# Optimization experiments

Measured on AMD Instinct MI355X. Metric: run time of the kernel, lower is better.

## Reference

```python
import jax, jax.numpy as jnp
import numpy as np

B, CIN, COUT, K, STRIDE, PAD = 32, 64, 128, 3, 1, 1
IN_H, IN_W = 112, 112


def setup_inputs() -> dict:
    key = jax.random.key(0)
    k1, k2 = jax.random.split(key)
    # x_padded already has `PAD` rows/cols of zeros on each side, as in the torch module
    x = jax.random.normal(k1, (B, CIN, IN_H, IN_W), dtype=jnp.float32)
    x_padded = jnp.pad(x, ((0, 0), (0, 0), (PAD, PAD), (PAD, PAD)))
    weight = jax.random.normal(k2, (COUT, CIN, K, K), dtype=jnp.float32) * 0.1
    bias = jnp.zeros((COUT,), dtype=jnp.float32)
    return {
        "x_padded": x_padded,
        "in_height": IN_H,
        "in_width": IN_W,
        "weight": weight,
        "bias": bias,
    }


def reference(x_padded, in_height, in_width, weight, bias):
    # CustomConv2D.custom_conv2d: direct conv over the pre-padded input.
    # out[b,o,h,w] = sum_{i,kh,kw} x_padded[b,i,h*s+kh,w*s+kw] * weight[o,i,kh,kw] + bias[o]
    out = jax.lax.conv_general_dilated(
        x_padded, weight,
        window_strides=(STRIDE, STRIDE),
        padding="VALID",  # padding already applied to x_padded
        dimension_numbers=("NCHW", "OIHW", "NCHW"),
    )
    return out + bias[None, :, None, None]
```

## Files before the change

kernel.cpp:

```cpp
#include <hip/hip_runtime.h>

typedef __attribute__((ext_vector_type(8))) short short8;
typedef __attribute__((ext_vector_type(4))) float f32x4;
typedef __attribute__((ext_vector_type(4))) unsigned int u32x4;
typedef unsigned short u16;
typedef unsigned int u32;

#define XH 114
#define XW 114
#define CINC 64
#define COUT 128
#define OH 112
#define OW 112
#define NB 32
#define KTOT 576
#define ROWB 14592

static __device__ __forceinline__ u16 f2bf(float f) {
    u32 x = __float_as_uint(f);
    u32 r = (x + 0x7fffu + ((x >> 16) & 1u)) >> 16;
    return (u16)r;
}

#define MFMA16(a, b, c) __builtin_amdgcn_mfma_f32_16x16x32_bf16((a), (b), (c), 0, 0, 0)

static __device__ __forceinline__ void gload16(const void* g, void* l) {
    __builtin_amdgcn_global_load_lds(
        (const __attribute__((address_space(1))) unsigned int*)g,
        (__attribute__((address_space(3))) unsigned int*)l, 16, 0, 0);
}


__global__ __launch_bounds__(256) void prep(const float* __restrict__ x,
                                            const float* __restrict__ w,
                                            u16* __restrict__ xb,
                                            u16* __restrict__ wbf) {
    const int tid = threadIdx.x;
    const int blk = blockIdx.x;
    if (blk >= NB * XH) {
        int i = (blk - NB * XH) * 256 + tid;
        int o = i / KTOT;
        int rem = i - o * KTOT;
        int khkw = rem >> 6;
        int ci = rem & 63;
        wbf[i] = f2bf(w[(o * CINC + ci) * 9 + khkw]);
        return;
    }
    __shared__ u16 tile[XW * 70];
    const int b = blk / XH;
    const int h = blk - b * XH;

    #pragma unroll
    for (int it = 0; it < 15; ++it) {
        int idx = it * 256 + tid;
        if (idx < 32 * XW) {
            int cp = idx / XW;
            int w_ = idx - cp * XW;
            const float* s0 = x + ((size_t)(b * CINC + 2 * cp) * XH + h) * XW + w_;
            float a = s0[0];
            float c = s0[XH * XW];
            u32 pk = (u32)f2bf(a) | ((u32)f2bf(c) << 16);
            *(u32*)&tile[w_ * 70 + 2 * cp] = pk;
        }
    }
    __syncthreads();

    u16* dstrow = xb + (size_t)(b * XH + h) * (XW * CINC);
    #pragma unroll
    for (int p2 = 0; p2 < 4; ++p2) {
        int task = p2 * 256 + tid;
        if (task < XW * 8) {
            int w_ = task >> 3;
            int c8 = task & 7;
            const u32* s = (const u32*)&tile[w_ * 70 + c8 * 8];
            u32x4 v = {s[0], s[1], s[2], s[3]};
            int slot = c8 ^ ((2 * h + w_) & 7);
            *(u32x4*)(dstrow + w_ * CINC + slot * 8) = v;
        }
    }
}

__global__ __launch_bounds__(256, 2) void conv_ring(const u16* __restrict__ xb,
                                                    const u16* __restrict__ wbf,
                                                    const float* __restrict__ bias,
                                                    float* __restrict__ out) {
    __shared__ u16 lds[4 * XW * CINC];
    char* ldsc = (char*)lds;

    const int tid  = threadIdx.x;
    const int lane = tid & 63;
    const int wv   = tid >> 6;
    const int l16  = lane & 15;
    const int lhi  = lane >> 4;

    int bidx = blockIdx.x;
    { int xcd = bidx & 7; bidx = xcd * 64 + (bidx >> 3); }
    const int bb = bidx >> 4;
    const int h0 = (bidx & 15) * 7;

    const u16* wrow0 = wbf + (wv * 32 + l16) * KTOT + lhi * 8;
    const u16* wrow1 = wrow0 + 16 * KTOT;
    short8 areg0[18], areg1[18];
    #pragma unroll
    for (int t = 0; t < 18; ++t) {
        areg0[t] = *(const short8*)(wrow0 + t * 32);
        areg1[t] = *(const short8*)(wrow1 + t * 32);
    }
    const float bv0 = bias[wv * 32 + l16];
    const float bv1 = bias[wv * 32 + 16 + l16];

    auto STAGE = [&](int hin) {
        const char* src = (const char*)(xb + (size_t)(bb * XH + hin) * (XW * CINC));
        char* dst = ldsc + (hin & 3) * ROWB;
        #pragma unroll
        for (int it = 0; it < 4; ++it) {
            const int c = it * 4 + wv;
            const int off = c * 1024;
            if (c < 14) {
                gload16(src + off + lane * 16, dst + off);
            } else if (c == 14) {
                if (lane < 16) gload16(src + off + lane * 16, dst + off);
            }
        }
    };

    STAGE(h0); STAGE(h0 + 1); STAGE(h0 + 2);
    __builtin_amdgcn_sched_barrier(0);
    asm volatile("s_waitcnt vmcnt(0) lgkmcnt(0)" ::: "memory");
    __builtin_amdgcn_sched_barrier(0);
    __builtin_amdgcn_s_barrier();

    const f32x4 zero = {0.f, 0.f, 0.f, 0.f};

    #pragma unroll 1
    for (int i = 0; i < 7; ++i) {
        const int hrow = h0 + i;
        if (i < 6) STAGE(hrow + 3);

        f32x4 acc[2][7];
        #pragma unroll
        for (int mf = 0; mf < 2; ++mf)
            #pragma unroll
            for (int nf = 0; nf < 7; ++nf) acc[mf][nf] = zero;

        #pragma unroll
        for (int tt = 0; tt < 9; ++tt) {
            const int kh = tt / 3;
            const int kw = tt - kh * 3;
            const int hin = hrow + kh;
            const int sb  = (hin & 3) * ROWB;
            const int hash = (2 * hin + kw + l16) & 7;
            const int ba0 = sb + ((kw + l16) << 7) + ((lhi ^ hash) << 4);

            #pragma unroll
            for (int nf = 0; nf < 7; ++nf) {
                short8 bf = *(const short8*)(ldsc + ba0 + nf * 2048);
                acc[0][nf] = MFMA16(bf, areg0[2 * tt], acc[0][nf]);
                acc[1][nf] = MFMA16(bf, areg1[2 * tt], acc[1][nf]);
            }
            #pragma unroll
            for (int nf = 0; nf < 7; ++nf) {
                short8 bf = *(const short8*)(ldsc + (ba0 ^ 0x40) + nf * 2048);
                acc[0][nf] = MFMA16(bf, areg0[2 * tt + 1], acc[0][nf]);
                acc[1][nf] = MFMA16(bf, areg1[2 * tt + 1], acc[1][nf]);
            }
        }

        #pragma unroll
        for (int mf = 0; mf < 2; ++mf) {
            const int o = wv * 32 + mf * 16 + l16;
            const float bv = mf ? bv1 : bv0;
            float* po = out + ((size_t)bb * COUT + o) * (OH * OW) + hrow * OW;
            #pragma unroll
            for (int nf = 0; nf < 7; ++nf) {
                f32x4 v = acc[mf][nf];
                v[0] += bv; v[1] += bv; v[2] += bv; v[3] += bv;
                *(f32x4*)(po + nf * 16 + lhi * 4) = v;
            }
        }

        __builtin_amdgcn_sched_barrier(0);
        asm volatile("s_waitcnt vmcnt(14) lgkmcnt(0)" ::: "memory");
        __builtin_amdgcn_sched_barrier(0);
        __builtin_amdgcn_s_barrier();
    }
}


#define BK 32
#define NSTEP 18
#define LDB 40

__global__ __launch_bounds__(256) void wcvt_ident(const float* __restrict__ w,
                                                  u16* __restrict__ wbf) {
    int i = blockIdx.x * 256 + threadIdx.x;
    if (i < COUT * KTOT) wbf[i] = f2bf(w[i]);
}

__global__ __launch_bounds__(256) void conv_fb(const float* __restrict__ x,
                                               const u16* __restrict__ wbf,
                                               const float* __restrict__ bias,
                                               float* __restrict__ out) {
    __shared__ u16 ldsB[OW * LDB];
    const int tid = threadIdx.x;
    int bid = blockIdx.x;
    { int xcd = bid & 7; bid = xcd * 448 + (bid >> 3); }
    const int b = bid / OH;
    const int h = bid - b * OH;
    const float* xbp = x + (size_t)b * (CINC * XH * XW);
    float* outb = out + (size_t)b * (COUT * OH * OW) + h * OW;
    const int lane = tid & 63, wv = tid >> 6, l16 = lane & 15, lhi = lane >> 4;
    const int m0 = wv * 32;
    const int sk = tid >> 3, sn0 = (tid & 7) * 14;
    f32x4 acc[2][7];
    const f32x4 zero = {0.f, 0.f, 0.f, 0.f};
    #pragma unroll
    for (int i = 0; i < 2; ++i)
        #pragma unroll
        for (int j = 0; j < 7; ++j) acc[i][j] = zero;
    for (int t = 0; t < NSTEP; ++t) {
        const int kg = t * BK + sk;
        const int ci = kg / 9;
        const int r9 = kg - ci * 9;
        const int kh = r9 / 3, kw = r9 - (r9 / 3) * 3;
        const float* src = xbp + ((size_t)ci * XH + (h + kh)) * XW + kw + sn0;
        __syncthreads();
        #pragma unroll
        for (int i = 0; i < 14; ++i) ldsB[(sn0 + i) * LDB + sk] = f2bf(src[i]);
        __syncthreads();
        short8 afrag[2];
        #pragma unroll
        for (int mf = 0; mf < 2; ++mf)
            afrag[mf] = *(const short8*)(wbf + (m0 + mf * 16 + l16) * KTOT + t * BK + lhi * 8);
        #pragma unroll
        for (int nf = 0; nf < 7; ++nf) {
            short8 bfrag = *(const short8*)&ldsB[(nf * 16 + l16) * LDB + lhi * 8];
            acc[0][nf] = MFMA16(afrag[0], bfrag, acc[0][nf]);
            acc[1][nf] = MFMA16(afrag[1], bfrag, acc[1][nf]);
        }
    }
    #pragma unroll
    for (int mf = 0; mf < 2; ++mf)
        #pragma unroll
        for (int j = 0; j < 4; ++j) {
            const int o = m0 + mf * 16 + lhi * 4 + j;
            const float bv = bias[o];
            #pragma unroll
            for (int nf = 0; nf < 7; ++nf)
                outb[(size_t)o * (OH * OW) + nf * 16 + l16] = acc[mf][nf][j] + bv;
        }
}

extern "C" void kernel_launch(void* const* d_in, const int* in_sizes, int n_in,
                              void* d_out, int out_size, void* d_ws, size_t ws_size,
                              hipStream_t stream) {
    const float* x    = (const float*)d_in[0];
    const float* w    = (const float*)d_in[3];
    const float* bias = (const float*)d_in[4];
    float* out = (float*)d_out;

    const size_t WBYTES = (size_t)COUT * KTOT * 2;
    const size_t XBYTES = (size_t)NB * XH * XW * CINC * 2;
    if (ws_size >= WBYTES + XBYTES) {
        u16* wbf = (u16*)d_ws;
        u16* xb  = (u16*)((char*)d_ws + WBYTES);
        prep<<<NB * XH + (COUT * KTOT) / 256, 256, 0, stream>>>(x, w, xb, wbf);
        conv_ring<<<512, 256, 0, stream>>>(xb, wbf, bias, out);
    } else {
        u16* wbf = (u16*)d_ws;
        wcvt_ident<<<(COUT * KTOT + 255) / 256, 256, 0, stream>>>(w, wbf);
        conv_fb<<<NB * OH, 256, 0, stream>>>(x, wbf, bias, out);
    }
}
```

Baseline: 110.5 us.

## Shrink LDS ring to three rows and split rows across more blocks

Reduces the LDS row ring from four buffers to three by issuing the next row's load after the kh=0 phase finishes reading the oldest buffer, guarded by an extra barrier. The grid grows from 512 to 768 blocks, each handling 5 or 4 output rows instead of 7, to improve load balance across CUs and let smaller LDS use raise occupancy. The cost is an extra barrier per output row, more redundant halo row loads and weight register preloads per block, and modulo-3 indexing.

```diff
diff --git a/kernel.cpp b/kernel.cpp
--- a/kernel.cpp
+++ b/kernel.cpp
@@ -80,11 +80,11 @@
     }
 }
 
-__global__ __launch_bounds__(256, 2) void conv_ring(const u16* __restrict__ xb,
-                                                    const u16* __restrict__ wbf,
-                                                    const float* __restrict__ bias,
-                                                    float* __restrict__ out) {
-    __shared__ u16 lds[4 * XW * CINC];
+__global__ __launch_bounds__(256, 2) void conv_ring3(const u16* __restrict__ xb,
+                                                     const u16* __restrict__ wbf,
+                                                     const float* __restrict__ bias,
+                                                     float* __restrict__ out) {
+    __shared__ u16 lds[3 * XW * CINC];
     char* ldsc = (char*)lds;
 
     const int tid  = threadIdx.x;
@@ -94,9 +94,11 @@
     const int lhi  = lane >> 4;
 
     int bidx = blockIdx.x;
-    { int xcd = bidx & 7; bidx = xcd * 64 + (bidx >> 3); }
-    const int bb = bidx >> 4;
-    const int h0 = (bidx & 15) * 7;
+    { int xcd = bidx & 7; bidx = xcd * 96 + (bidx >> 3); }
+    const int bb  = bidx / 24;
+    const int grp = bidx - bb * 24;
+    const int h0  = grp < 16 ? grp * 5 : 80 + (grp - 16) * 4;
+    const int cnt = grp < 16 ? 5 : 4;
 
     const u16* wrow0 = wbf + (wv * 32 + l16) * KTOT + lhi * 8;
     const u16* wrow1 = wrow0 + 16 * KTOT;
@@ -111,7 +113,7 @@
 
     auto STAGE = [&](int hin) {
         const char* src = (const char*)(xb + (size_t)(bb * XH + hin) * (XW * CINC));
-        char* dst = ldsc + (hin & 3) * ROWB;
+        char* dst = ldsc + (hin % 3) * ROWB;
         #pragma unroll
         for (int it = 0; it < 4; ++it) {
             const int c = it * 4 + wv;
@@ -133,9 +135,8 @@
     const f32x4 zero = {0.f, 0.f, 0.f, 0.f};
 
     #pragma unroll 1
-    for (int i = 0; i < 7; ++i) {
+    for (int i = 0; i < cnt; ++i) {
         const int hrow = h0 + i;
-        if (i < 6) STAGE(hrow + 3);
 
         f32x4 acc[2][7];
         #pragma unroll
@@ -143,28 +144,39 @@
             #pragma unroll
             for (int nf = 0; nf < 7; ++nf) acc[mf][nf] = zero;
 
-        #pragma unroll
-        for (int tt = 0; tt < 9; ++tt) {
-            const int kh = tt / 3;
-            const int kw = tt - kh * 3;
+        auto PHASE = [&](int kh) {
             const int hin = hrow + kh;
-            const int sb  = (hin & 3) * ROWB;
-            const int hash = (2 * hin + kw + l16) & 7;
-            const int ba0 = sb + ((kw + l16) << 7) + ((lhi ^ hash) << 4);
-
-            #pragma unroll
-            for (int nf = 0; nf < 7; ++nf) {
-                short8 bf = *(const short8*)(ldsc + ba0 + nf * 2048);
-                acc[0][nf] = MFMA16(bf, areg0[2 * tt], acc[0][nf]);
-                acc[1][nf] = MFMA16(bf, areg1[2 * tt], acc[1][nf]);
+            const int sb  = (hin % 3) * ROWB;
+            #pragma unroll
+            for (int kw = 0; kw < 3; ++kw) {
+                const int tt = kh * 3 + kw;
+                const int hash = (2 * hin + kw + l16) & 7;
+                const int ba0 = sb + ((kw + l16) << 7) + ((lhi ^ hash) << 4);
+                #pragma unroll
+                for (int nf = 0; nf < 7; ++nf) {
+                    short8 bf = *(const short8*)(ldsc + ba0 + nf * 2048);
+                    acc[0][nf] = MFMA16(bf, areg0[2 * tt], acc[0][nf]);
+                    acc[1][nf] = MFMA16(bf, areg1[2 * tt], acc[1][nf]);
+                }
+                #pragma unroll
+                for (int nf = 0; nf < 7; ++nf) {
+                    short8 bf = *(const short8*)(ldsc + (ba0 ^ 0x40) + nf * 2048);
+                    acc[0][nf] = MFMA16(bf, areg0[2 * tt + 1], acc[0][nf]);
+                    acc[1][nf] = MFMA16(bf, areg1[2 * tt + 1], acc[1][nf]);
+                }
             }
-            #pragma unroll
-            for (int nf = 0; nf < 7; ++nf) {
-                short8 bf = *(const short8*)(ldsc + (ba0 ^ 0x40) + nf * 2048);
-                acc[0][nf] = MFMA16(bf, areg0[2 * tt + 1], acc[0][nf]);
-                acc[1][nf] = MFMA16(bf, areg1[2 * tt + 1], acc[1][nf]);
-            }
-        }
+        };
+
+        PHASE(0);
+
+        __builtin_amdgcn_sched_barrier(0);
+        asm volatile("s_waitcnt lgkmcnt(0)" ::: "memory");
+        __builtin_amdgcn_sched_barrier(0);
+        __builtin_amdgcn_s_barrier();
+        if (i < cnt - 1) STAGE(hrow + 3);
+
+        PHASE(1);
+        PHASE(2);
 
         #pragma unroll
         for (int mf = 0; mf < 2; ++mf) {
@@ -265,7 +277,7 @@
         u16* wbf = (u16*)d_ws;
         u16* xb  = (u16*)((char*)d_ws + WBYTES);
         prep<<<NB * XH + (COUT * KTOT) / 256, 256, 0, stream>>>(x, w, xb, wbf);
-        conv_ring<<<512, 256, 0, stream>>>(xb, wbf, bias, out);
+        conv_ring3<<<768, 256, 0, stream>>>(xb, wbf, bias, out);
     } else {
         u16* wbf = (u16*)d_ws;
         wcvt_ident<<<(COUT * KTOT + 255) / 256, 256, 0, stream>>>(w, wbf);
```

Measured after the change: 125.6 us. +13.7%, slower.

## Fuse fp32-to-bf16 NHWC input conversion into conv kernel, drop prep pass

Applied to the files above, without the earlier changes.

Removes the separate prep kernel that wrote a bf16 channel-last, swizzled copy of the input to workspace. The conv kernel now loads fp32 NCHW rows directly into registers, converts them to bf16 and writes them swizzled into the LDS ring. The next row's global loads are issued before the MFMA loop and stored to LDS after it, so load latency overlaps compute. This avoids the intermediate global write and re-read, at the cost of more VGPRs, more scattered 4-byte LDS stores, and conversion ALU work inside the conv kernel.

```diff
diff --git a/kernel.cpp b/kernel.cpp
--- a/kernel.cpp
+++ b/kernel.cpp
@@ -2,7 +2,6 @@
 
 typedef __attribute__((ext_vector_type(8))) short short8;
 typedef __attribute__((ext_vector_type(4))) float f32x4;
-typedef __attribute__((ext_vector_type(4))) unsigned int u32x4;
 typedef unsigned short u16;
 typedef unsigned int u32;
 
@@ -24,63 +23,17 @@
 
 #define MFMA16(a, b, c) __builtin_amdgcn_mfma_f32_16x16x32_bf16((a), (b), (c), 0, 0, 0)
 
-static __device__ __forceinline__ void gload16(const void* g, void* l) {
-    __builtin_amdgcn_global_load_lds(
-        (const __attribute__((address_space(1))) unsigned int*)g,
-        (__attribute__((address_space(3))) unsigned int*)l, 16, 0, 0);
-}
-
-
-__global__ __launch_bounds__(256) void prep(const float* __restrict__ x,
-                                            const float* __restrict__ w,
-                                            u16* __restrict__ xb,
-                                            u16* __restrict__ wbf) {
-    const int tid = threadIdx.x;
-    const int blk = blockIdx.x;
-    if (blk >= NB * XH) {
-        int i = (blk - NB * XH) * 256 + tid;
-        int o = i / KTOT;
-        int rem = i - o * KTOT;
-        int khkw = rem >> 6;
-        int ci = rem & 63;
-        wbf[i] = f2bf(w[(o * CINC + ci) * 9 + khkw]);
-        return;
-    }
-    __shared__ u16 tile[XW * 70];
-    const int b = blk / XH;
-    const int h = blk - b * XH;
-
-    #pragma unroll
-    for (int it = 0; it < 15; ++it) {
-        int idx = it * 256 + tid;
-        if (idx < 32 * XW) {
-            int cp = idx / XW;
-            int w_ = idx - cp * XW;
-            const float* s0 = x + ((size_t)(b * CINC + 2 * cp) * XH + h) * XW + w_;
-            float a = s0[0];
-            float c = s0[XH * XW];
-            u32 pk = (u32)f2bf(a) | ((u32)f2bf(c) << 16);
-            *(u32*)&tile[w_ * 70 + 2 * cp] = pk;
-        }
-    }
-    __syncthreads();
-
-    u16* dstrow = xb + (size_t)(b * XH + h) * (XW * CINC);
-    #pragma unroll
-    for (int p2 = 0; p2 < 4; ++p2) {
-        int task = p2 * 256 + tid;
-        if (task < XW * 8) {
-            int w_ = task >> 3;
-            int c8 = task & 7;
-            const u32* s = (const u32*)&tile[w_ * 70 + c8 * 8];
-            u32x4 v = {s[0], s[1], s[2], s[3]};
-            int slot = c8 ^ ((2 * h + w_) & 7);
-            *(u32x4*)(dstrow + w_ * CINC + slot * 8) = v;
-        }
-    }
-}
-
-__global__ __launch_bounds__(256, 2) void conv_ring(const u16* __restrict__ xb,
+__global__ __launch_bounds__(256) void wcvt_reord(const float* __restrict__ w,
+                                                  u16* __restrict__ wbf) {
+    int i = blockIdx.x * 256 + threadIdx.x;
+    int o = i / KTOT;
+    int rem = i - o * KTOT;
+    int khkw = rem >> 6;
+    int ci = rem & 63;
+    wbf[i] = f2bf(w[(o * CINC + ci) * 9 + khkw]);
+}
+
+__global__ __launch_bounds__(256, 2) void conv_fuse(const float* __restrict__ x,
                                                     const u16* __restrict__ wbf,
                                                     const float* __restrict__ bias,
                                                     float* __restrict__ out) {
@@ -97,6 +50,12 @@
     { int xcd = bidx & 7; bidx = xcd * 64 + (bidx >> 3); }
     const int bb = bidx >> 4;
     const int h0 = (bidx & 15) * 7;
+
+    const int scp = tid & 31;
+    const int sws = tid >> 5;
+    const float* xbase = x + ((size_t)(bb * CINC + 2 * scp) * XH) * XW + sws * 16;
+    const int slotb = scp >> 2;
+    const int cilo  = ((2 * scp) & 7) << 1;
 
     const u16* wrow0 = wbf + (wv * 32 + l16) * KTOT + lhi * 8;
     const u16* wrow1 = wrow0 + 16 * KTOT;
@@ -109,25 +68,41 @@
     const float bv0 = bias[wv * 32 + l16];
     const float bv1 = bias[wv * 32 + 16 + l16];
 
-    auto STAGE = [&](int hin) {
-        const char* src = (const char*)(xb + (size_t)(bb * XH + hin) * (XW * CINC));
+    #pragma unroll 1
+    for (int r = 0; r < 3; ++r) {
+        const int hin = h0 + r;
+        const float* p0 = xbase + (size_t)hin * XW;
+        const float* p1 = p0 + XH * XW;
         char* dst = ldsc + (hin & 3) * ROWB;
-        #pragma unroll
-        for (int it = 0; it < 4; ++it) {
-            const int c = it * 4 + wv;
-            const int off = c * 1024;
-            if (c < 14) {
-                gload16(src + off + lane * 16, dst + off);
-            } else if (c == 14) {
-                if (lane < 16) gload16(src + off + lane * 16, dst + off);
-            }
-        }
-    };
-
-    STAGE(h0); STAGE(h0 + 1); STAGE(h0 + 2);
-    __builtin_amdgcn_sched_barrier(0);
-    asm volatile("s_waitcnt vmcnt(0) lgkmcnt(0)" ::: "memory");
-    __builtin_amdgcn_sched_barrier(0);
+        const int hb = 2 * hin;
+        if (sws < 7) {
+            f32x4 s0[4], s1[4];
+            #pragma unroll
+            for (int k = 0; k < 4; ++k) { s0[k] = *(const f32x4*)(p0 + k * 4);
+                                          s1[k] = *(const f32x4*)(p1 + k * 4); }
+            asm volatile("s_waitcnt vmcnt(0)" ::: "memory");
+            #pragma unroll
+            for (int k = 0; k < 4; ++k)
+                #pragma unroll
+                for (int e = 0; e < 4; ++e) {
+                    const int w = sws * 16 + k * 4 + e;
+                    u32 pk = (u32)f2bf(s0[k][e]) | ((u32)f2bf(s1[k][e]) << 16);
+                    const int swz = slotb ^ ((hb + w) & 7);
+                    *(u32*)(dst + ((w << 7) | (swz << 4) | cilo)) = pk;
+                }
+        } else {
+            float a0 = p0[0], a1 = p0[1], b0_ = p1[0], b1_ = p1[1];
+            asm volatile("s_waitcnt vmcnt(0)" ::: "memory");
+            #pragma unroll
+            for (int e = 0; e < 2; ++e) {
+                const int w = 112 + e;
+                u32 pk = (u32)f2bf(e ? a1 : a0) | ((u32)f2bf(e ? b1_ : b0_) << 16);
+                const int swz = slotb ^ ((hb + w) & 7);
+                *(u32*)(dst + ((w << 7) | (swz << 4) | cilo)) = pk;
+            }
+        }
+    }
+    asm volatile("s_waitcnt lgkmcnt(0)" ::: "memory");
     __builtin_amdgcn_s_barrier();
 
     const f32x4 zero = {0.f, 0.f, 0.f, 0.f};
@@ -135,7 +110,21 @@
     #pragma unroll 1
     for (int i = 0; i < 7; ++i) {
         const int hrow = h0 + i;
-        if (i < 6) STAGE(hrow + 3);
+
+        f32x4 s0[4], s1[4];
+        float ta0 = 0.f, ta1 = 0.f, tb0 = 0.f, tb1 = 0.f;
+        if (i < 6) {
+            const float* p0 = xbase + (size_t)(hrow + 3) * XW;
+            const float* p1 = p0 + XH * XW;
+            if (sws < 7) {
+                #pragma unroll
+                for (int k = 0; k < 4; ++k) { s0[k] = *(const f32x4*)(p0 + k * 4);
+                                              s1[k] = *(const f32x4*)(p1 + k * 4); }
+            } else {
+                ta0 = p0[0]; ta1 = p0[1]; tb0 = p1[0]; tb1 = p1[1];
+            }
+        }
+        __builtin_amdgcn_sched_barrier(0);
 
         f32x4 acc[2][7];
         #pragma unroll
@@ -144,25 +133,52 @@
             for (int nf = 0; nf < 7; ++nf) acc[mf][nf] = zero;
 
         #pragma unroll
-        for (int tt = 0; tt < 9; ++tt) {
-            const int kh = tt / 3;
-            const int kw = tt - kh * 3;
+        for (int kh = 0; kh < 3; ++kh) {
             const int hin = hrow + kh;
             const int sb  = (hin & 3) * ROWB;
-            const int hash = (2 * hin + kw + l16) & 7;
-            const int ba0 = sb + ((kw + l16) << 7) + ((lhi ^ hash) << 4);
-
-            #pragma unroll
-            for (int nf = 0; nf < 7; ++nf) {
-                short8 bf = *(const short8*)(ldsc + ba0 + nf * 2048);
-                acc[0][nf] = MFMA16(bf, areg0[2 * tt], acc[0][nf]);
-                acc[1][nf] = MFMA16(bf, areg1[2 * tt], acc[1][nf]);
-            }
-            #pragma unroll
-            for (int nf = 0; nf < 7; ++nf) {
-                short8 bf = *(const short8*)(ldsc + (ba0 ^ 0x40) + nf * 2048);
-                acc[0][nf] = MFMA16(bf, areg0[2 * tt + 1], acc[0][nf]);
-                acc[1][nf] = MFMA16(bf, areg1[2 * tt + 1], acc[1][nf]);
+            #pragma unroll
+            for (int kw = 0; kw < 3; ++kw) {
+                const int tt = kh * 3 + kw;
+                const int hash = (2 * hin + kw + l16) & 7;
+                const int ba0 = sb + ((kw + l16) << 7) + ((lhi ^ hash) << 4);
+                #pragma unroll
+                for (int nf = 0; nf < 7; ++nf) {
+                    short8 bf = *(const short8*)(ldsc + ba0 + nf * 2048);
+                    acc[0][nf] = MFMA16(bf, areg0[2 * tt], acc[0][nf]);
+                    acc[1][nf] = MFMA16(bf, areg1[2 * tt], acc[1][nf]);
+                }
+                #pragma unroll
+                for (int nf = 0; nf < 7; ++nf) {
+                    short8 bf = *(const short8*)(ldsc + (ba0 ^ 0x40) + nf * 2048);
+                    acc[0][nf] = MFMA16(bf, areg0[2 * tt + 1], acc[0][nf]);
+                    acc[1][nf] = MFMA16(bf, areg1[2 * tt + 1], acc[1][nf]);
+                }
+            }
+        }
+
+        asm volatile("s_waitcnt vmcnt(0)" ::: "memory");
+        if (i < 6) {
+            const int hin = hrow + 3;
+            char* dst = ldsc + (hin & 3) * ROWB;
+            const int hb = 2 * hin;
+            if (sws < 7) {
+                #pragma unroll
+                for (int k = 0; k < 4; ++k)
+                    #pragma unroll
+                    for (int e = 0; e < 4; ++e) {
+                        const int w = sws * 16 + k * 4 + e;
+                        u32 pk = (u32)f2bf(s0[k][e]) | ((u32)f2bf(s1[k][e]) << 16);
+                        const int swz = slotb ^ ((hb + w) & 7);
+                        *(u32*)(dst + ((w << 7) | (swz << 4) | cilo)) = pk;
+                    }
+            } else {
+                #pragma unroll
+                for (int e = 0; e < 2; ++e) {
+                    const int w = 112 + e;
+                    u32 pk = (u32)f2bf(e ? ta1 : ta0) | ((u32)f2bf(e ? tb1 : tb0) << 16);
+                    const int swz = slotb ^ ((hb + w) & 7);
+                    *(u32*)(dst + ((w << 7) | (swz << 4) | cilo)) = pk;
+                }
             }
         }
 
@@ -180,7 +196,7 @@
         }
 
         __builtin_amdgcn_sched_barrier(0);
-        asm volatile("s_waitcnt vmcnt(14) lgkmcnt(0)" ::: "memory");
+        asm volatile("s_waitcnt lgkmcnt(0)" ::: "memory");
         __builtin_amdgcn_sched_barrier(0);
         __builtin_amdgcn_s_barrier();
     }
@@ -260,12 +276,10 @@
     float* out = (float*)d_out;
 
     const size_t WBYTES = (size_t)COUT * KTOT * 2;
-    const size_t XBYTES = (size_t)NB * XH * XW * CINC * 2;
-    if (ws_size >= WBYTES + XBYTES) {
+    if (ws_size >= WBYTES) {
         u16* wbf = (u16*)d_ws;
-        u16* xb  = (u16*)((char*)d_ws + WBYTES);
-        prep<<<NB * XH + (COUT * KTOT) / 256, 256, 0, stream>>>(x, w, xb, wbf);
-        conv_ring<<<512, 256, 0, stream>>>(xb, wbf, bias, out);
+        wcvt_reord<<<(COUT * KTOT) / 256, 256, 0, stream>>>(w, wbf);
+        conv_fuse<<<512, 256, 0, stream>>>(x, wbf, bias, out);
     } else {
         u16* wbf = (u16*)d_ws;
         wcvt_ident<<<(COUT * KTOT + 255) / 256, 256, 0, stream>>>(w, wbf);
```

New measurement: 166.3 us. 1.51x slower.

## Fuse input bf16 conversion into conv kernel via per-block private halo buffer

Applied to the files above, without the earlier changes.

Adds a conv_fus9 kernel in which each block converts its own 9 input rows (7 output rows plus halo) from fp32 NCHW into a swizzled bf16 NHWC layout, writes them to a per-block private workspace region, and then streams them into the LDS ring, as the existing conv_ring does. This removes the separate full-tensor prep pass and its global round trip for the converted input. The cost is that halo rows are converted twice by neighbouring blocks, the conversion sits serially before the MFMA loop in each block, and more workspace is needed. The conv_ring tap loop is also restructured into nested kh/kw loops, which is a cosmetic change.

```diff
diff --git a/kernel.cpp b/kernel.cpp
--- a/kernel.cpp
+++ b/kernel.cpp
@@ -15,6 +15,7 @@
 #define NB 32
 #define KTOT 576
 #define ROWB 14592
+#define PRIVB (9 * ROWB)
 
 static __device__ __forceinline__ u16 f2bf(float f) {
     u32 x = __float_as_uint(f);
@@ -28,6 +29,162 @@
     __builtin_amdgcn_global_load_lds(
         (const __attribute__((address_space(1))) unsigned int*)g,
         (__attribute__((address_space(3))) unsigned int*)l, 16, 0, 0);
+}
+
+__global__ __launch_bounds__(256) void wcvt_reord(const float* __restrict__ w,
+                                                  u16* __restrict__ wbf) {
+    int i = blockIdx.x * 256 + threadIdx.x;
+    int o = i / KTOT;
+    int rem = i - o * KTOT;
+    int khkw = rem >> 6;
+    int ci = rem & 63;
+    wbf[i] = f2bf(w[(o * CINC + ci) * 9 + khkw]);
+}
+
+__global__ __launch_bounds__(256, 2) void conv_fus9(const float* __restrict__ x,
+                                                    const u16* __restrict__ wbf,
+                                                    u16* __restrict__ priv,
+                                                    const float* __restrict__ bias,
+                                                    float* __restrict__ out) {
+    __shared__ u16 lds[4 * XW * CINC];
+    __shared__ u16 tile[XW * 70];
+    char* ldsc = (char*)lds;
+
+    const int tid  = threadIdx.x;
+    const int lane = tid & 63;
+    const int wv   = tid >> 6;
+    const int l16  = lane & 15;
+    const int lhi  = lane >> 4;
+
+    int bidx = blockIdx.x;
+    { int xcd = bidx & 7; bidx = xcd * 64 + (bidx >> 3); }
+    const int bb = bidx >> 4;
+    const int h0 = (bidx & 15) * 7;
+
+    u16* myxb = priv + (size_t)bidx * (PRIVB / 2);
+
+    #pragma unroll 1
+    for (int r = 0; r < 9; ++r) {
+        const int hin = h0 + r;
+        #pragma unroll
+        for (int it = 0; it < 15; ++it) {
+            int idx = it * 256 + tid;
+            if (idx < 32 * XW) {
+                int cp = idx / XW;
+                int w_ = idx - cp * XW;
+                const float* s0 = x + ((size_t)(bb * CINC + 2 * cp) * XH + hin) * XW + w_;
+                float a = s0[0];
+                float c = s0[XH * XW];
+                u32 pk = (u32)f2bf(a) | ((u32)f2bf(c) << 16);
+                *(u32*)&tile[w_ * 70 + 2 * cp] = pk;
+            }
+        }
+        __syncthreads();
+        u16* dstrow = myxb + (size_t)r * (ROWB / 2);
+        #pragma unroll
+        for (int p2 = 0; p2 < 4; ++p2) {
+            int task = p2 * 256 + tid;
+            if (task < XW * 8) {
+                int w_ = task >> 3;
+                int c8 = task & 7;
+                const u32* s = (const u32*)&tile[w_ * 70 + c8 * 8];
+                u32x4 v = {s[0], s[1], s[2], s[3]};
+                int slot = c8 ^ ((2 * hin + w_) & 7);
+                *(u32x4*)(dstrow + w_ * CINC + slot * 8) = v;
+            }
+        }
+        __syncthreads();
+    }
+    asm volatile("s_waitcnt vmcnt(0)" ::: "memory");
+    __builtin_amdgcn_s_barrier();
+
+    const u16* wrow0 = wbf + (wv * 32 + l16) * KTOT + lhi * 8;
+    const u16* wrow1 = wrow0 + 16 * KTOT;
+    short8 areg0[18], areg1[18];
+    #pragma unroll
+    for (int t = 0; t < 18; ++t) {
+        areg0[t] = *(const short8*)(wrow0 + t * 32);
+        areg1[t] = *(const short8*)(wrow1 + t * 32);
+    }
+    const float bv0 = bias[wv * 32 + l16];
+    const float bv1 = bias[wv * 32 + 16 + l16];
+
+    auto STAGE = [&](int hin) {
+        const char* src = (const char*)myxb + (size_t)(hin - h0) * ROWB;
+        char* dst = ldsc + (hin & 3) * ROWB;
+        #pragma unroll
+        for (int it = 0; it < 4; ++it) {
+            const int c = it * 4 + wv;
+            const int off = c * 1024;
+            if (c < 14) {
+                gload16(src + off + lane * 16, dst + off);
+            } else if (c == 14) {
+                if (lane < 16) gload16(src + off + lane * 16, dst + off);
+            }
+        }
+    };
+
+    STAGE(h0); STAGE(h0 + 1); STAGE(h0 + 2);
+    __builtin_amdgcn_sched_barrier(0);
+    asm volatile("s_waitcnt vmcnt(0) lgkmcnt(0)" ::: "memory");
+    __builtin_amdgcn_sched_barrier(0);
+    __builtin_amdgcn_s_barrier();
+
+    const f32x4 zero = {0.f, 0.f, 0.f, 0.f};
+
+    #pragma unroll 1
+    for (int i = 0; i < 7; ++i) {
+        const int hrow = h0 + i;
+        if (i < 6) STAGE(hrow + 3);
+
+        f32x4 acc[2][7];
+        #pragma unroll
+        for (int mf = 0; mf < 2; ++mf)
+            #pragma unroll
+            for (int nf = 0; nf < 7; ++nf) acc[mf][nf] = zero;
+
+        #pragma unroll
+        for (int kh = 0; kh < 3; ++kh) {
+            const int hin = hrow + kh;
+            const int sb  = (hin & 3) * ROWB;
+            #pragma unroll
+            for (int kw = 0; kw < 3; ++kw) {
+                const int tt = kh * 3 + kw;
+                const int hash = (2 * hin + kw + l16) & 7;
+                const int ba0 = sb + ((kw + l16) << 7) + ((lhi ^ hash) << 4);
+                #pragma unroll
+                for (int nf = 0; nf < 7; ++nf) {
+                    short8 bf = *(const short8*)(ldsc + ba0 + nf * 2048);
+                    acc[0][nf] = MFMA16(bf, areg0[2 * tt], acc[0][nf]);
+                    acc[1][nf] = MFMA16(bf, areg1[2 * tt], acc[1][nf]);
+                }
+                #pragma unroll
+                for (int nf = 0; nf < 7; ++nf) {
+                    short8 bf = *(const short8*)(ldsc + (ba0 ^ 0x40) + nf * 2048);
+                    acc[0][nf] = MFMA16(bf, areg0[2 * tt + 1], acc[0][nf]);
+                    acc[1][nf] = MFMA16(bf, areg1[2 * tt + 1], acc[1][nf]);
+                }
+            }
+        }
+
+        #pragma unroll
+        for (int mf = 0; mf < 2; ++mf) {
+            const int o = wv * 32 + mf * 16 + l16;
+            const float bv = mf ? bv1 : bv0;
+            float* po = out + ((size_t)bb * COUT + o) * (OH * OW) + hrow * OW;
+            #pragma unroll
+            for (int nf = 0; nf < 7; ++nf) {
+                f32x4 v = acc[mf][nf];
+                v[0] += bv; v[1] += bv; v[2] += bv; v[3] += bv;
+                *(f32x4*)(po + nf * 16 + lhi * 4) = v;
+            }
+        }
+
+        __builtin_amdgcn_sched_barrier(0);
+        asm volatile("s_waitcnt vmcnt(14) lgkmcnt(0)" ::: "memory");
+        __builtin_amdgcn_sched_barrier(0);
+        __builtin_amdgcn_s_barrier();
+    }
 }
 
 
@@ -144,25 +301,26 @@
             for (int nf = 0; nf < 7; ++nf) acc[mf][nf] = zero;
 
         #pragma unroll
-        for (int tt = 0; tt < 9; ++tt) {
-            const int kh = tt / 3;
-            const int kw = tt - kh * 3;
+        for (int kh = 0; kh < 3; ++kh) {
             const int hin = hrow + kh;
             const int sb  = (hin & 3) * ROWB;
-            const int hash = (2 * hin + kw + l16) & 7;
-            const int ba0 = sb + ((kw + l16) << 7) + ((lhi ^ hash) << 4);
-
-            #pragma unroll
-            for (int nf = 0; nf < 7; ++nf) {
-                short8 bf = *(const short8*)(ldsc + ba0 + nf * 2048);
-                acc[0][nf] = MFMA16(bf, areg0[2 * tt], acc[0][nf]);
-                acc[1][nf] = MFMA16(bf, areg1[2 * tt], acc[1][nf]);
-            }
-            #pragma unroll
-            for (int nf = 0; nf < 7; ++nf) {
-                short8 bf = *(const short8*)(ldsc + (ba0 ^ 0x40) + nf * 2048);
-                acc[0][nf] = MFMA16(bf, areg0[2 * tt + 1], acc[0][nf]);
-                acc[1][nf] = MFMA16(bf, areg1[2 * tt + 1], acc[1][nf]);
+            #pragma unroll
+            for (int kw = 0; kw < 3; ++kw) {
+                const int tt = kh * 3 + kw;
+                const int hash = (2 * hin + kw + l16) & 7;
+                const int ba0 = sb + ((kw + l16) << 7) + ((lhi ^ hash) << 4);
+                #pragma unroll
+                for (int nf = 0; nf < 7; ++nf) {
+                    short8 bf = *(const short8*)(ldsc + ba0 + nf * 2048);
+                    acc[0][nf] = MFMA16(bf, areg0[2 * tt], acc[0][nf]);
+                    acc[1][nf] = MFMA16(bf, areg1[2 * tt], acc[1][nf]);
+                }
+                #pragma unroll
+                for (int nf = 0; nf < 7; ++nf) {
+                    short8 bf = *(const short8*)(ldsc + (ba0 ^ 0x40) + nf * 2048);
+                    acc[0][nf] = MFMA16(bf, areg0[2 * tt + 1], acc[0][nf]);
+                    acc[1][nf] = MFMA16(bf, areg1[2 * tt + 1], acc[1][nf]);
+                }
             }
         }
 
@@ -261,7 +419,14 @@
 
     const size_t WBYTES = (size_t)COUT * KTOT * 2;
     const size_t XBYTES = (size_t)NB * XH * XW * CINC * 2;
-    if (ws_size >= WBYTES + XBYTES) {
+    const size_t PBYTES = (size_t)512 * PRIVB;
+
+    if (ws_size >= WBYTES + PBYTES) {
+        u16* wbf  = (u16*)d_ws;
+        u16* priv = (u16*)((char*)d_ws + WBYTES);
+        wcvt_reord<<<(COUT * KTOT) / 256, 256, 0, stream>>>(w, wbf);
+        conv_fus9<<<512, 256, 0, stream>>>(x, wbf, priv, bias, out);
+    } else if (ws_size >= WBYTES + XBYTES) {
         u16* wbf = (u16*)d_ws;
         u16* xb  = (u16*)((char*)d_ws + WBYTES);
         prep<<<NB * XH + (COUT * KTOT) / 256, 256, 0, stream>>>(x, w, xb, wbf);
```

Measured after the change: 138.1 us. 25.0% more time.
